# Kernel tuning notes

Hardware: AMD Instinct MI355X
Metric: run time of the kernel (lower is better)

The kernel has to match this reference:

```python
import jax, jax.numpy as jnp
import numpy as np
from jax import lax

DN = ('NCHW', 'OIHW', 'NCHW')


def setup_inputs() -> dict:
    key = jax.random.key(0)
    ks = jax.random.split(key, 5)
    B, C, H, W = 1, 128, 64, 64
    heads = 4
    return {
        'x_q': jax.random.normal(ks[0], (B, C, H, W), jnp.float32),
        'x_kv': jax.random.normal(ks[1], (B, C, H, W), jnp.float32),
        'w_qkv': jax.random.normal(ks[2], (3 * C, C, 1, 1), jnp.float32) * 0.05,
        'w_dw': jax.random.normal(ks[3], (3 * C, 1, 3, 3), jnp.float32) * 0.2,
        'w_proj': jax.random.normal(ks[4], (C, C, 1, 1), jnp.float32) * 0.05,
        'temperature': jnp.ones((heads, 1, 1), jnp.float32),
    }


def reference(x_q, x_kv, w_qkv, w_dw, w_proj, temperature):
    B, C, H, W = x_q.shape
    heads = temperature.shape[0]
    hd = C // heads
    N = H * W

    # shared qkv 1x1 conv + depthwise 3x3 conv on concatenated [2B,C,H,W]
    x = jnp.concatenate([x_q, x_kv], axis=0)
    qkv = lax.conv_general_dilated(x, w_qkv, (1, 1), 'VALID', dimension_numbers=DN)
    qkv = lax.conv_general_dilated(qkv, w_dw, (1, 1), 'SAME',
                                   feature_group_count=3 * C, dimension_numbers=DN)
    q, k, v = jnp.split(qkv, 3, axis=1)
    q = q[:B]          # query branch from x_q
    k = k[B:]          # key/value branch from x_kv
    v = v[B:]

    def to_heads(t):   # [B,C,H,W] -> [B,h,N,d]
        return t.reshape(B, heads, hd, N).transpose(0, 1, 3, 2)

    attn = jnp.einsum('bhnd,bhmd->bhnm', to_heads(q), to_heads(k)) * temperature
    attn = jax.nn.softmax(attn, axis=-1)
    out = jnp.einsum('bhnm,bhmd->bhnd', attn, to_heads(v))
    out = out.transpose(0, 1, 3, 2).reshape(B, C, H, W)
    return lax.conv_general_dilated(out, w_proj, (1, 1), 'VALID', dimension_numbers=DN)
```

## Files before the change

kernel.cpp:

```cpp
#include <hip/hip_runtime.h>

typedef short bf16x4 __attribute__((ext_vector_type(4)));
typedef short bf16x8 __attribute__((ext_vector_type(8)));
typedef float f32x4 __attribute__((ext_vector_type(4)));
typedef unsigned short u16x4 __attribute__((ext_vector_type(4)));
typedef unsigned short u16x8 __attribute__((ext_vector_type(8)));

__device__ __forceinline__ unsigned short f2bf(float f) {
  union { float f; unsigned u; } v; v.f = f;
  unsigned r = v.u + 0x7FFFu + ((v.u >> 16) & 1u);
  return (unsigned short)(r >> 16);
}
__device__ __forceinline__ unsigned fbits(float f) {
  union { float f; unsigned u; } x; x.f = f; return x.u;
}
__device__ __forceinline__ float bfloat(unsigned u) {
  union { unsigned u; float f; } x; x.u = u; return x.f;
}
__device__ __forceinline__ float fexp2(float x) {
#if __has_builtin(__builtin_amdgcn_exp2f)
  return __builtin_amdgcn_exp2f(x);
#else
  return exp2f(x);
#endif
}
__device__ __forceinline__ f32x4 pv_mfma(bf16x4 a, bf16x4 b, f32x4 c) {
#if __has_builtin(__builtin_amdgcn_mfma_f32_16x16x16bf16_1k)
  return __builtin_amdgcn_mfma_f32_16x16x16bf16_1k(a, b, c, 0, 0, 0);
#else
  bf16x8 az = {a[0], a[1], a[2], a[3], 0, 0, 0, 0};
  bf16x8 bz = {b[0], b[1], b[2], b[3], 0, 0, 0, 0};
  return __builtin_amdgcn_mfma_f32_16x16x32_bf16(az, bz, c, 0, 0, 0);
#endif
}

__global__ __launch_bounds__(256)
void cast_kernel(const float* __restrict__ Xq, const float* __restrict__ Xkv,
                 const float* __restrict__ Wqkv, const float* __restrict__ Wproj,
                 unsigned short* __restrict__ XT, unsigned short* __restrict__ Wq16,
                 unsigned short* __restrict__ Wph, unsigned short* __restrict__ Wpl)
{
  const int b = blockIdx.x, t = threadIdx.x;
  if (b < 256) {
    __shared__ __align__(16) float Tl[64][68];
    const int img = b >> 7, kt = (b >> 6) & 1, nt = b & 63;
    const float* X = img ? Xkv : Xq;
    #pragma unroll
    for (int i = 0; i < 4; ++i) {
      int e = i * 256 + t;
      int r = e >> 4, c4 = (e & 15) * 4;
      *(f32x4*)&Tl[r][c4] = *(const f32x4*)&X[(kt * 64 + r) * 4096 + nt * 64 + c4];
    }
    __syncthreads();
    unsigned short* out = XT + img * (4096 * 128);
    #pragma unroll
    for (int i = 0; i < 2; ++i) {
      int u = i * 256 + t;
      int n = u >> 3, kg = u & 7;
      u16x8 tv;
      #pragma unroll
      for (int j = 0; j < 8; ++j) tv[j] = f2bf(Tl[kg * 8 + j][n]);
      *(u16x8*)&out[(nt * 64 + n) * 128 + kt * 64 + kg * 8] = tv;
    }
  } else {
    const int wb = b - 256;
    if (wb < 3) {
      #pragma unroll 4
      for (int i = 0; i < 64; ++i) {
        int idx = wb * 16384 + i * 256 + t;
        Wq16[idx] = f2bf(Wqkv[idx]);
      }
    } else {
      #pragma unroll 4
      for (int i = 0; i < 64; ++i) {
        int idx = i * 256 + t;
        float v = Wproj[idx];
        unsigned short h = f2bf(v);
        float hf = bfloat((unsigned)h << 16);
        Wph[idx] = h;
        Wpl[idx] = f2bf(v - hf);
      }
    }
  }
}

__global__ __launch_bounds__(256)
void gemm_qkv_kernel(const unsigned short* __restrict__ XT,
                     const unsigned short* __restrict__ Wq16, float* __restrict__ Y)
{
  const int t = threadIdx.x;
  const int w = t >> 6, c = t & 15, g = (t & 63) >> 4;
  const int n0 = blockIdx.x * 32;
  const int ob = blockIdx.y;
  const int o_base = ob * 64 + w * 16;
  const unsigned short* B = XT + (ob >= 2 ? 4096 * 128 : 0);
  f32x4 acc0 = {0.f, 0.f, 0.f, 0.f}, acc1 = {0.f, 0.f, 0.f, 0.f};
  #pragma unroll
  for (int ks = 0; ks < 4; ++ks) {
    bf16x8 a = *(const bf16x8*)&Wq16[(o_base + c) * 128 + ks * 32 + g * 8];
    bf16x8 b0 = *(const bf16x8*)&B[(n0 + c) * 128 + ks * 32 + g * 8];
    bf16x8 b1 = *(const bf16x8*)&B[(n0 + 16 + c) * 128 + ks * 32 + g * 8];
    acc0 = __builtin_amdgcn_mfma_f32_16x16x32_bf16(a, b0, acc0, 0, 0, 0);
    acc1 = __builtin_amdgcn_mfma_f32_16x16x32_bf16(a, b1, acc1, 0, 0, 0);
  }
  #pragma unroll
  for (int i = 0; i < 4; ++i) {
    Y[(o_base + 4 * g + i) * 4096 + n0 + c] = acc0[i];
    Y[(o_base + 4 * g + i) * 4096 + n0 + 16 + c] = acc1[i];
  }
}

__global__ __launch_bounds__(256)
void gemm_proj_kernel(const unsigned short* __restrict__ Oth,
                      const unsigned short* __restrict__ Otl,
                      const unsigned short* __restrict__ Wph,
                      const unsigned short* __restrict__ Wpl, float* __restrict__ Y)
{
  const int t = threadIdx.x;
  const int w = t >> 6, c = t & 15, g = (t & 63) >> 4;
  const int n0 = blockIdx.x * 32;
  const int o_base = blockIdx.y * 64 + w * 16;
  f32x4 acc0 = {0.f, 0.f, 0.f, 0.f}, acc1 = {0.f, 0.f, 0.f, 0.f};
  #pragma unroll
  for (int ks = 0; ks < 4; ++ks) {
    const int ko = ks * 32 + g * 8;
    bf16x8 ah = *(const bf16x8*)&Wph[(o_base + c) * 128 + ko];
    bf16x8 al = *(const bf16x8*)&Wpl[(o_base + c) * 128 + ko];
    bf16x8 bh0 = *(const bf16x8*)&Oth[(n0 + c) * 128 + ko];
    bf16x8 bl0 = *(const bf16x8*)&Otl[(n0 + c) * 128 + ko];
    bf16x8 bh1 = *(const bf16x8*)&Oth[(n0 + 16 + c) * 128 + ko];
    bf16x8 bl1 = *(const bf16x8*)&Otl[(n0 + 16 + c) * 128 + ko];
    acc0 = __builtin_amdgcn_mfma_f32_16x16x32_bf16(al, bh0, acc0, 0, 0, 0);
    acc0 = __builtin_amdgcn_mfma_f32_16x16x32_bf16(ah, bl0, acc0, 0, 0, 0);
    acc0 = __builtin_amdgcn_mfma_f32_16x16x32_bf16(ah, bh0, acc0, 0, 0, 0);
    acc1 = __builtin_amdgcn_mfma_f32_16x16x32_bf16(al, bh1, acc1, 0, 0, 0);
    acc1 = __builtin_amdgcn_mfma_f32_16x16x32_bf16(ah, bl1, acc1, 0, 0, 0);
    acc1 = __builtin_amdgcn_mfma_f32_16x16x32_bf16(ah, bh1, acc1, 0, 0, 0);
  }
  #pragma unroll
  for (int i = 0; i < 4; ++i) {
    Y[(o_base + 4 * g + i) * 4096 + n0 + c] = acc0[i];
    Y[(o_base + 4 * g + i) * 4096 + n0 + 16 + c] = acc1[i];
  }
}

__global__ __launch_bounds__(256)
void dwconv_kernel(const float* __restrict__ T, const float* __restrict__ Wd,
                   const float* __restrict__ temp, unsigned short* __restrict__ Qb)
{
  __shared__ __align__(16) float P[4096];
  const int jc = blockIdx.x;
  const int t = threadIdx.x;
  const float* in = T + jc * 4096;
  #pragma unroll
  for (int i = 0; i < 4; ++i)
    *(f32x4*)&P[(i * 256 + t) * 4] = *(const f32x4*)&in[(i * 256 + t) * 4];
  float w[9];
  #pragma unroll
  for (int k = 0; k < 9; ++k) w[k] = Wd[jc * 9 + k];
  const float scale = (jc < 128) ? temp[jc >> 5] * 1.4426950408889634f : 1.0f;
  __syncthreads();
  unsigned short* out = Qb + jc * 4096;
  #pragma unroll 4
  for (int i = 0; i < 16; ++i) {
    int idx = i * 256 + t;
    int y = idx >> 6, x = idx & 63;
    float acc = 0.f;
    #pragma unroll
    for (int dy = -1; dy <= 1; ++dy) {
      int yy = y + dy;
      if (yy < 0 || yy > 63) continue;
      #pragma unroll
      for (int dx = -1; dx <= 1; ++dx) {
        int xx = x + dx;
        if (xx < 0 || xx > 63) continue;
        acc += w[(dy + 1) * 3 + (dx + 1)] * P[yy * 64 + xx];
      }
    }
    out[idx] = f2bf(acc * scale);
  }
}

#define KOFF (128 * 4096)
#define VOFF (256 * 4096)
#define KSTR 40
#define VSTR 132

__global__ __launch_bounds__(1024, 4)
void attn_kernel(const unsigned short* __restrict__ Qb,
                 unsigned short* __restrict__ Oth, unsigned short* __restrict__ Otl)
{
  __shared__ __align__(16) char lds[74752];
  unsigned short* Kg = (unsigned short*)lds;
  unsigned short* Vg = (unsigned short*)(lds + 40960);
  const int t = threadIdx.x;
  const int g4 = t >> 8;
  const int ts = t & 255;
  const int qw = (t >> 6) & 3;
  const int l = t & 63;
  const int c = l & 15, g = l >> 4;
  const int h = blockIdx.y;
  const int nq = blockIdx.x * 64 + qw * 16;

  unsigned short* Kgg = Kg + g4 * (128 * KSTR);
  unsigned short* Vgg = Vg + g4 * (32 * VSTR);

  bf16x8 qf;
  #pragma unroll
  for (int e = 0; e < 8; ++e)
    qf[e] = (short)Qb[(h * 32 + g * 8 + e) * 4096 + nq + c];

  f32x4 oh0 = {0.f, 0.f, 0.f, 0.f}, oh1 = {0.f, 0.f, 0.f, 0.f};
  float lsum = 0.f;

  const int kdp = ts >> 4;
  const int kj  = ts & 15;
  const int vdd = ts >> 4;
  const int vj  = ts & 15;

  u16x4 kr0[2], kr1[2];
  u16x8 vr[2];
  {
    const int m0 = g4 * 128;
    #pragma unroll
    for (int it = 0; it < 2; ++it) {
      int m = kj * 4 + it * 64;
      kr0[it] = *(const u16x4*)&Qb[KOFF + (h * 32 + 2 * kdp) * 4096 + m0 + m];
      kr1[it] = *(const u16x4*)&Qb[KOFF + (h * 32 + 2 * kdp + 1) * 4096 + m0 + m];
      vr[it] = *(const u16x8*)&Qb[VOFF + (h * 32 + vdd + 16 * it) * 4096 + m0 + vj * 8];
    }
  }

  for (int tt = 0; tt < 8; ++tt) {
    __syncthreads();
    #pragma unroll
    for (int it = 0; it < 2; ++it) {
      int m = kj * 4 + it * 64;
      #pragma unroll
      for (int i = 0; i < 4; ++i)
        *(unsigned*)&Kgg[(m + i) * KSTR + 2 * kdp] =
            (unsigned)kr0[it][i] | ((unsigned)kr1[it][i] << 16);
      int d = vdd + 16 * it;
      *(u16x4*)&Vgg[d * VSTR + vj * 8] =
          __builtin_shufflevector(vr[it], vr[it], 0, 1, 2, 3);
      *(u16x4*)&Vgg[d * VSTR + vj * 8 + 4] =
          __builtin_shufflevector(vr[it], vr[it], 4, 5, 6, 7);
    }
    __syncthreads();
    if (tt < 7) {
      const int m0n = ((tt + 1) * 4 + g4) * 128;
      #pragma unroll
      for (int it = 0; it < 2; ++it) {
        int m = kj * 4 + it * 64;
        kr0[it] = *(const u16x4*)&Qb[KOFF + (h * 32 + 2 * kdp) * 4096 + m0n + m];
        kr1[it] = *(const u16x4*)&Qb[KOFF + (h * 32 + 2 * kdp + 1) * 4096 + m0n + m];
        vr[it] = *(const u16x8*)&Qb[VOFF + (h * 32 + vdd + 16 * it) * 4096 + m0n + vj * 8];
      }
    }
    #pragma unroll
    for (int j = 0; j < 8; ++j) {
      bf16x8 kf = *(const bf16x8*)&Kgg[(j * 16 + c) * KSTR + g * 8];
      f32x4 z = {0.f, 0.f, 0.f, 0.f};
      f32x4 s = __builtin_amdgcn_mfma_f32_16x16x32_bf16(kf, qf, z, 0, 0, 0);

      unsigned u0 = fbits(fexp2(s[0]));
      unsigned u1 = fbits(fexp2(s[1]));
      unsigned u2 = fbits(fexp2(s[2]));
      unsigned u3 = fbits(fexp2(s[3]));
      unsigned t0 = u0 & 0xFFFF0000u, t1 = u1 & 0xFFFF0000u;
      unsigned t2 = u2 & 0xFFFF0000u, t3 = u3 & 0xFFFF0000u;
      lsum += (bfloat(t0) + bfloat(t1)) + (bfloat(t2) + bfloat(t3));
      unsigned pk0 = (u0 >> 16) | t1;
      unsigned pk1 = (u2 >> 16) | t3;
      union { unsigned u[2]; bf16x4 v; } pu;
      pu.u[0] = pk0; pu.u[1] = pk1;

      bf16x4 vf0 = *(const bf16x4*)&Vgg[c * VSTR + j * 16 + g * 4];
      bf16x4 vf1 = *(const bf16x4*)&Vgg[(16 + c) * VSTR + j * 16 + g * 4];
      oh0 = pv_mfma(vf0, pu.v, oh0);
      oh1 = pv_mfma(vf1, pu.v, oh1);
    }
  }

  lsum += __shfl_xor(lsum, 16, 64);
  lsum += __shfl_xor(lsum, 32, 64);

  __syncthreads();
  float* Of = (float*)lds;
  float* lf = (float*)(lds + 36864);
  #pragma unroll
  for (int r = 0; r < 4; ++r) {
    Of[(g4 * 32 + 4 * g + r) * 66 + qw * 16 + c]      = oh0[r];
    Of[(g4 * 32 + 16 + 4 * g + r) * 66 + qw * 16 + c] = oh1[r];
  }
  if (l < 16) lf[g4 * 64 + qw * 16 + c] = lsum;
  __syncthreads();

  #pragma unroll
  for (int e = t; e < 2048; e += 1024) {
    int d = e & 31, q = e >> 5;
    float s4 = Of[(0 * 32 + d) * 66 + q] + Of[(1 * 32 + d) * 66 + q] +
               Of[(2 * 32 + d) * 66 + q] + Of[(3 * 32 + d) * 66 + q];
    float li = lf[q] + lf[64 + q] + lf[128 + q] + lf[192 + q];
    float val = s4 / li;
    unsigned short hi = f2bf(val);
    float hf = bfloat((unsigned)hi << 16);
    int idx = (blockIdx.x * 64 + q) * 128 + h * 32 + d;
    Oth[idx] = hi;
    Otl[idx] = f2bf(val - hf);
  }
}

extern "C" void kernel_launch(void* const* d_in, const int* in_sizes, int n_in,
                              void* d_out, int out_size, void* d_ws, size_t ws_size,
                              hipStream_t stream) {
  const float* xq    = (const float*)d_in[0];
  const float* xkv   = (const float*)d_in[1];
  const float* wqkv  = (const float*)d_in[2];
  const float* wdw   = (const float*)d_in[3];
  const float* wproj = (const float*)d_in[4];
  const float* temp  = (const float*)d_in[5];
  float* out = (float*)d_out;

  char* ws = (char*)d_ws;
  float* t_pre        = (float*)ws;
  unsigned short* qb  = (unsigned short*)(ws + 6291456);
  unsigned short* xt  = (unsigned short*)(ws + 9437184);
  unsigned short* wq16= (unsigned short*)(ws + 11534336);
  unsigned short* wph = (unsigned short*)(ws + 11632640);
  unsigned short* wpl = (unsigned short*)(ws + 11665408);
  unsigned short* oth = (unsigned short*)(ws + 11698176);
  unsigned short* otl = (unsigned short*)(ws + 12746752);

  cast_kernel<<<dim3(260), 256, 0, stream>>>(xq, xkv, wqkv, wproj, xt, wq16, wph, wpl);
  gemm_qkv_kernel<<<dim3(128, 6), 256, 0, stream>>>(xt, wq16, t_pre);
  dwconv_kernel<<<dim3(384), 256, 0, stream>>>(t_pre, wdw, temp, qb);
  attn_kernel<<<dim3(64, 4), 1024, 0, stream>>>(qb, oth, otl);
  gemm_proj_kernel<<<dim3(128, 2), 256, 0, stream>>>(oth, otl, wph, wpl, out);
}
```

Before: 60.74 us.

## Store qkv intermediate in bf16 and let each attention wave cover all queries

The qkv GEMM now writes its output in bf16 instead of fp32, and the depthwise conv reads and widens it. This halves the intermediate traffic but rounds the data before the conv. In the attention kernel, each wave now handles all four 16-query sub-tiles against a quarter of the key tile. The K and V fragments loaded from LDS are reused across four MFMAs instead of one. The cost is four times the accumulator registers and a serialized per-wave LDS reduction with extra barriers at the end.

```diff
diff --git a/kernel.cpp b/kernel.cpp
--- a/kernel.cpp
+++ b/kernel.cpp
@@ -86,7 +86,8 @@
 
 __global__ __launch_bounds__(256)
 void gemm_qkv_kernel(const unsigned short* __restrict__ XT,
-                     const unsigned short* __restrict__ Wq16, float* __restrict__ Y)
+                     const unsigned short* __restrict__ Wq16,
+                     unsigned short* __restrict__ Y16)
 {
   const int t = threadIdx.x;
   const int w = t >> 6, c = t & 15, g = (t & 63) >> 4;
@@ -105,8 +106,8 @@
   }
   #pragma unroll
   for (int i = 0; i < 4; ++i) {
-    Y[(o_base + 4 * g + i) * 4096 + n0 + c] = acc0[i];
-    Y[(o_base + 4 * g + i) * 4096 + n0 + 16 + c] = acc1[i];
+    Y16[(o_base + 4 * g + i) * 4096 + n0 + c] = f2bf(acc0[i]);
+    Y16[(o_base + 4 * g + i) * 4096 + n0 + 16 + c] = f2bf(acc1[i]);
   }
 }
 
@@ -145,16 +146,20 @@
 }
 
 __global__ __launch_bounds__(256)
-void dwconv_kernel(const float* __restrict__ T, const float* __restrict__ Wd,
+void dwconv_kernel(const unsigned short* __restrict__ T16, const float* __restrict__ Wd,
                    const float* __restrict__ temp, unsigned short* __restrict__ Qb)
 {
   __shared__ __align__(16) float P[4096];
   const int jc = blockIdx.x;
   const int t = threadIdx.x;
-  const float* in = T + jc * 4096;
-  #pragma unroll
-  for (int i = 0; i < 4; ++i)
-    *(f32x4*)&P[(i * 256 + t) * 4] = *(const f32x4*)&in[(i * 256 + t) * 4];
+  const unsigned short* in = T16 + jc * 4096;
+  #pragma unroll
+  for (int i = 0; i < 2; ++i) {
+    u16x8 v = *(const u16x8*)&in[(i * 256 + t) * 8];
+    #pragma unroll
+    for (int j = 0; j < 8; ++j)
+      P[(i * 256 + t) * 8 + j] = bfloat((unsigned)v[j] << 16);
+  }
   float w[9];
   #pragma unroll
   for (int k = 0; k < 9; ++k) w[k] = Wd[jc * 9 + k];
@@ -200,18 +205,25 @@
   const int l = t & 63;
   const int c = l & 15, g = l >> 4;
   const int h = blockIdx.y;
-  const int nq = blockIdx.x * 64 + qw * 16;
+  const int nq = blockIdx.x * 64;
 
   unsigned short* Kgg = Kg + g4 * (128 * KSTR);
   unsigned short* Vgg = Vg + g4 * (32 * VSTR);
 
-  bf16x8 qf;
-  #pragma unroll
-  for (int e = 0; e < 8; ++e)
-    qf[e] = (short)Qb[(h * 32 + g * 8 + e) * 4096 + nq + c];
-
-  f32x4 oh0 = {0.f, 0.f, 0.f, 0.f}, oh1 = {0.f, 0.f, 0.f, 0.f};
-  float lsum = 0.f;
+  bf16x8 qf[4];
+  #pragma unroll
+  for (int s = 0; s < 4; ++s)
+    #pragma unroll
+    for (int e = 0; e < 8; ++e)
+      qf[s][e] = (short)Qb[(h * 32 + g * 8 + e) * 4096 + nq + s * 16 + c];
+
+  f32x4 oh[4][2];
+  #pragma unroll
+  for (int s = 0; s < 4; ++s) {
+    oh[s][0] = (f32x4){0.f, 0.f, 0.f, 0.f};
+    oh[s][1] = (f32x4){0.f, 0.f, 0.f, 0.f};
+  }
+  float lsum[4] = {0.f, 0.f, 0.f, 0.f};
 
   const int kdp = ts >> 4;
   const int kj  = ts & 15;
@@ -258,51 +270,76 @@
       }
     }
     #pragma unroll
-    for (int j = 0; j < 8; ++j) {
+    for (int jj = 0; jj < 2; ++jj) {
+      const int j = qw * 2 + jj;
       bf16x8 kf = *(const bf16x8*)&Kgg[(j * 16 + c) * KSTR + g * 8];
-      f32x4 z = {0.f, 0.f, 0.f, 0.f};
-      f32x4 s = __builtin_amdgcn_mfma_f32_16x16x32_bf16(kf, qf, z, 0, 0, 0);
-
-      unsigned u0 = fbits(fexp2(s[0]));
-      unsigned u1 = fbits(fexp2(s[1]));
-      unsigned u2 = fbits(fexp2(s[2]));
-      unsigned u3 = fbits(fexp2(s[3]));
-      unsigned t0 = u0 & 0xFFFF0000u, t1 = u1 & 0xFFFF0000u;
-      unsigned t2 = u2 & 0xFFFF0000u, t3 = u3 & 0xFFFF0000u;
-      lsum += (bfloat(t0) + bfloat(t1)) + (bfloat(t2) + bfloat(t3));
-      unsigned pk0 = (u0 >> 16) | t1;
-      unsigned pk1 = (u2 >> 16) | t3;
-      union { unsigned u[2]; bf16x4 v; } pu;
-      pu.u[0] = pk0; pu.u[1] = pk1;
-
       bf16x4 vf0 = *(const bf16x4*)&Vgg[c * VSTR + j * 16 + g * 4];
       bf16x4 vf1 = *(const bf16x4*)&Vgg[(16 + c) * VSTR + j * 16 + g * 4];
-      oh0 = pv_mfma(vf0, pu.v, oh0);
-      oh1 = pv_mfma(vf1, pu.v, oh1);
-    }
-  }
-
-  lsum += __shfl_xor(lsum, 16, 64);
-  lsum += __shfl_xor(lsum, 32, 64);
+      #pragma unroll
+      for (int s = 0; s < 4; ++s) {
+        f32x4 z = {0.f, 0.f, 0.f, 0.f};
+        f32x4 sv = __builtin_amdgcn_mfma_f32_16x16x32_bf16(kf, qf[s], z, 0, 0, 0);
+        unsigned u0 = fbits(fexp2(sv[0]));
+        unsigned u1 = fbits(fexp2(sv[1]));
+        unsigned u2 = fbits(fexp2(sv[2]));
+        unsigned u3 = fbits(fexp2(sv[3]));
+        unsigned t0 = u0 & 0xFFFF0000u, t1 = u1 & 0xFFFF0000u;
+        unsigned t2 = u2 & 0xFFFF0000u, t3 = u3 & 0xFFFF0000u;
+        lsum[s] += (bfloat(t0) + bfloat(t1)) + (bfloat(t2) + bfloat(t3));
+        unsigned pk0 = (u0 >> 16) | t1;
+        unsigned pk1 = (u2 >> 16) | t3;
+        union { unsigned u[2]; bf16x4 v; } pu;
+        pu.u[0] = pk0; pu.u[1] = pk1;
+        oh[s][0] = pv_mfma(vf0, pu.v, oh[s][0]);
+        oh[s][1] = pv_mfma(vf1, pu.v, oh[s][1]);
+      }
+    }
+  }
+
+  #pragma unroll
+  for (int s = 0; s < 4; ++s) {
+    lsum[s] += __shfl_xor(lsum[s], 16, 64);
+    lsum[s] += __shfl_xor(lsum[s], 32, 64);
+  }
 
   __syncthreads();
-  float* Of = (float*)lds;
-  float* lf = (float*)(lds + 36864);
-  #pragma unroll
+  float* OG  = (float*)lds;
+  float* lfq = (float*)(lds + 34048);
+  float* lf  = (float*)(lds + 36864);
+  if (l < 16) {
+    #pragma unroll
+    for (int s = 0; s < 4; ++s)
+      lf[(g4 * 4 + qw) * 64 + s * 16 + c] = lsum[s];
+  }
   for (int r = 0; r < 4; ++r) {
-    Of[(g4 * 32 + 4 * g + r) * 66 + qw * 16 + c]      = oh0[r];
-    Of[(g4 * 32 + 16 + 4 * g + r) * 66 + qw * 16 + c] = oh1[r];
-  }
-  if (l < 16) lf[g4 * 64 + qw * 16 + c] = lsum;
+    if (qw == r) {
+      #pragma unroll
+      for (int s = 0; s < 4; ++s)
+        #pragma unroll
+        for (int i = 0; i < 4; ++i) {
+          int d0 = 4 * g + i;
+          float* p0 = &OG[g4 * 2112 + d0 * 66 + s * 16 + c];
+          float* p1 = &OG[g4 * 2112 + (16 + d0) * 66 + s * 16 + c];
+          if (r == 0) { *p0 = oh[s][0][i];  *p1 = oh[s][1][i]; }
+          else        { *p0 += oh[s][0][i]; *p1 += oh[s][1][i]; }
+        }
+    }
+    __syncthreads();
+  }
+  if (t < 64) {
+    float a = 0.f;
+    #pragma unroll
+    for (int ww = 0; ww < 16; ++ww) a += lf[ww * 64 + t];
+    lfq[t] = a;
+  }
   __syncthreads();
 
   #pragma unroll
   for (int e = t; e < 2048; e += 1024) {
     int d = e & 31, q = e >> 5;
-    float s4 = Of[(0 * 32 + d) * 66 + q] + Of[(1 * 32 + d) * 66 + q] +
-               Of[(2 * 32 + d) * 66 + q] + Of[(3 * 32 + d) * 66 + q];
-    float li = lf[q] + lf[64 + q] + lf[128 + q] + lf[192 + q];
-    float val = s4 / li;
+    float s4 = OG[0 * 2112 + d * 66 + q] + OG[1 * 2112 + d * 66 + q] +
+               OG[2 * 2112 + d * 66 + q] + OG[3 * 2112 + d * 66 + q];
+    float val = s4 / lfq[q];
     unsigned short hi = f2bf(val);
     float hf = bfloat((unsigned)hi << 16);
     int idx = (blockIdx.x * 64 + q) * 128 + h * 32 + d;
@@ -323,18 +360,18 @@
   float* out = (float*)d_out;
 
   char* ws = (char*)d_ws;
-  float* t_pre        = (float*)ws;
-  unsigned short* qb  = (unsigned short*)(ws + 6291456);
-  unsigned short* xt  = (unsigned short*)(ws + 9437184);
-  unsigned short* wq16= (unsigned short*)(ws + 11534336);
-  unsigned short* wph = (unsigned short*)(ws + 11632640);
-  unsigned short* wpl = (unsigned short*)(ws + 11665408);
-  unsigned short* oth = (unsigned short*)(ws + 11698176);
-  unsigned short* otl = (unsigned short*)(ws + 12746752);
+  unsigned short* t16  = (unsigned short*)ws;
+  unsigned short* qb   = (unsigned short*)(ws + 3145728);
+  unsigned short* xt   = (unsigned short*)(ws + 6291456);
+  unsigned short* wq16 = (unsigned short*)(ws + 8388608);
+  unsigned short* wph  = (unsigned short*)(ws + 8486912);
+  unsigned short* wpl  = (unsigned short*)(ws + 8519680);
+  unsigned short* oth  = (unsigned short*)(ws + 8552448);
+  unsigned short* otl  = (unsigned short*)(ws + 9601024);
 
   cast_kernel<<<dim3(260), 256, 0, stream>>>(xq, xkv, wqkv, wproj, xt, wq16, wph, wpl);
-  gemm_qkv_kernel<<<dim3(128, 6), 256, 0, stream>>>(xt, wq16, t_pre);
-  dwconv_kernel<<<dim3(384), 256, 0, stream>>>(t_pre, wdw, temp, qb);
+  gemm_qkv_kernel<<<dim3(128, 6), 256, 0, stream>>>(xt, wq16, t16);
+  dwconv_kernel<<<dim3(384), 256, 0, stream>>>(t16, wdw, temp, qb);
   attn_kernel<<<dim3(64, 4), 1024, 0, stream>>>(qb, oth, otl);
   gemm_proj_kernel<<<dim3(128, 2), 256, 0, stream>>>(oth, otl, wph, wpl, out);
 }
```

Measured after the change: 62.34 us. 2.6% more time.
